# Performance work log

Measured on AMD Instinct MI355X. Metric: run time of the kernel, lower is better.

The kernel has to match this reference:

```python
import jax, jax.numpy as jnp
import numpy as np

N_POINTS = 1048576
N_LEVELS = 16
F = 2
BASE_RES = 16
FINEST_RES = 512
LOG2_HASH = 19
SIZES = [2 ** min(i + 1, LOG2_HASH) for i in range(N_LEVELS)]  # per-level table rows (powers of 2)
OFFS = np.concatenate([[0], np.cumsum(SIZES)]).astype(np.int64)  # static row offsets into packed table
TOTAL_ROWS = int(OFFS[-1])  # 131070
# hash primes from the torch module; uint32 wraparound matches int64 low-bit behavior
# because each table size is a power of two <= 2^19 < 2^32, so h % 2^k == low k bits.
P0, P1, P2, P3 = np.uint32(1), np.uint32(2654435761), np.uint32(29675113), np.uint32(123456789)
CORNERS = np.array([[0,0,0],[1,0,0],[0,1,0],[1,1,0],
                    [0,0,1],[1,0,1],[0,1,1],[1,1,1]], dtype=np.uint32)  # torch stacking order


def setup_inputs() -> dict:
    key = jax.random.key(0)
    k1, k2 = jax.random.split(key)
    coords = jax.random.uniform(k1, (N_POINTS, 3), dtype=jnp.float32, minval=-1.0, maxval=1.0)
    hash_init_scale = 0.001
    table = jax.random.uniform(k2, (TOTAL_ROWS, F), dtype=jnp.float32,
                               minval=-hash_init_scale, maxval=hash_init_scale)
    return {"coords": coords, "table": table}


def _encode(coords, table):
    corners = jnp.asarray(CORNERS)  # [8,3] uint32
    outs = []
    for level in range(N_LEVELS):
        res = min(BASE_RES * (2 ** level), FINEST_RES)
        cs = (coords + 1.0) * res           # [N,3]
        cf = jnp.floor(cs)
        frac = cs - cf                      # [N,3]
        base = cf.astype(jnp.uint32)        # coords >= -1 so floor >= 0
        c = base[None, :, :] + corners[:, None, :]   # [8,N,3]
        x, y, z = c[..., 0], c[..., 1], c[..., 2]
        h = x * P0
        h = h * P1 + y
        h = h * P2 + z
        h = h * P3
        h = (h & jnp.uint32(SIZES[level] - 1)).astype(jnp.int32)  # mod power-of-2 table size
        feats = table[int(OFFS[level]) + h]          # [8,N,F] gather
        tx = frac[..., 0:1]; ty = frac[..., 1:2]; tz = frac[..., 2:3]
        f = (feats[0] * (1 - tx) * (1 - ty) * (1 - tz)
             + feats[1] * tx * (1 - ty) * (1 - tz)
             + feats[2] * (1 - tx) * ty * (1 - tz)
             + feats[3] * tx * ty * (1 - tz)
             + feats[4] * (1 - tx) * (1 - ty) * tz
             + feats[5] * tx * (1 - ty) * tz
             + feats[6] * (1 - tx) * ty * tz
             + feats[7] * tx * ty * tz)              # [N,F]
        outs.append(f)
    return jnp.concatenate(outs, axis=-1)            # [N, N_LEVELS*F]


def reference(coords, table):
    return _encode(coords, table)
```

## Files before the change

### kernel.cpp

```cpp
#include <hip/hip_runtime.h>
#include <hip/hip_fp16.h>


#define BLOCK 1024
#define NBLOCKS 512
#define ITERS 16
#define STAGED_ROWS 32766
#define TBL_LDS_BYTES 131072
#define LDS_BYTES (TBL_LDS_BYTES + 16 * 128 * 8)

__device__ __forceinline__ float2 ldsRow(const unsigned* lds, unsigned idx) {
    unsigned u = lds[idx];
    __half2 h = *(__half2*)&u;
    return __half22float2(h);
}

#define PREP(FRES, HARR, WARR) \
    unsigned HARR[8]; float WARR[8]; { \
        const float csx = (px + 1.0f) * (FRES); \
        const float csy = (py + 1.0f) * (FRES); \
        const float csz = (pz + 1.0f) * (FRES); \
        const float cfx = floorf(csx), cfy = floorf(csy), cfz = floorf(csz); \
        const float tx = csx - cfx, ty = csy - cfy, tz = csz - cfz; \
        const unsigned hh = (unsigned)cfx * HA + (unsigned)cfy * HB + (unsigned)cfz * HC; \
        const float ux = 1.0f - tx, uy = 1.0f - ty, uz = 1.0f - tz; \
        WARR[0] = ux*uy*uz; WARR[1] = tx*uy*uz; WARR[2] = ux*ty*uz; WARR[3] = tx*ty*uz; \
        WARR[4] = ux*uy*tz; WARR[5] = tx*uy*tz; WARR[6] = ux*ty*tz; WARR[7] = tx*ty*tz; \
        HARR[0] = hh;           HARR[1] = hh + HA;           \
        HARR[2] = hh + HB;      HARR[3] = hh + HA + HB;      \
        HARR[4] = hh + HC;      HARR[5] = hh + HA + HC;      \
        HARR[6] = hh + HB + HC; HARR[7] = hh + HA + HB + HC; \
    }

#define GATHER_LDS(HARR, WARR, MASK, OFF, O0, O1) \
    { _Pragma("unroll") for (int c = 0; c < 8; ++c) { \
        float2 f = ldsRow(lds_tb, (OFF) + ((HARR[c]) & (MASK))); \
        (O0) += f.x * WARR[c]; (O1) += f.y * WARR[c]; } }

__global__ __launch_bounds__(BLOCK) void ngp_encode_kernel(
    const float* __restrict__ coords,
    const float* __restrict__ table,
    float* __restrict__ out)
{
    extern __shared__ unsigned char lds_raw[];
    unsigned* lds_tb = (unsigned*)lds_raw;
    float2* lds_t = (float2*)(lds_raw + TBL_LDS_BYTES);

    {
        const float4* __restrict__ t4 = (const float4*)table;
        uint2* __restrict__ l2 = (uint2*)lds_tb;
        for (int r = threadIdx.x; r < STAGED_ROWS / 2; r += BLOCK) {
            float4 v = t4[r];
            __half2 a = __floats2half2_rn(v.x, v.y);
            __half2 b = __floats2half2_rn(v.z, v.w);
            uint2 u;
            u.x = *(unsigned*)&a;
            u.y = *(unsigned*)&b;
            l2[r] = u;
        }
    }
    __syncthreads();

    constexpr unsigned P1 = 2654435761u, P2 = 29675113u, P3 = 123456789u;
    constexpr unsigned HA = P1 * P2 * P3;
    constexpr unsigned HB = P2 * P3;
    constexpr unsigned HC = P3;

    const float2* __restrict__ tb = (const float2*)table;
    float4* __restrict__ out4 = (float4*)out;

    const int wv   = __builtin_amdgcn_readfirstlane((int)(threadIdx.x >> 6));
    const int q    = wv & 7;
    const int g    = wv >> 3;
    const int lane = threadIdx.x & 63;
    const int pl   = g * 64 + lane;

    const int lA = q;
    const int lB = 15 - q;
    const unsigned maskA = (2u << lA) - 1u, offA = maskA - 1u;
    const unsigned maskB = (2u << lB) - 1u, offB = maskB - 1u;

    for (int it = 0; it < ITERS; ++it) {
        const int pbase = blockIdx.x * (ITERS * 128) + it * 128;
        const int p = pbase + pl;

        const float px = coords[3 * p + 0];
        const float py = coords[3 * p + 1];
        const float pz = coords[3 * p + 2];

        float oA0 = 0.0f, oA1 = 0.0f, oB0 = 0.0f, oB1 = 0.0f;

        if (q < 2) {
            PREP(512.0f, hB, wB)
            float2 gf0 = tb[offB + ((hB[0]) & maskB)];
            float2 gf1 = tb[offB + ((hB[1]) & maskB)];
            float2 gf2 = tb[offB + ((hB[2]) & maskB)];
            float2 gf3 = tb[offB + ((hB[3]) & maskB)];
            float2 gf4 = tb[offB + ((hB[4]) & maskB)];
            float2 gf5 = tb[offB + ((hB[5]) & maskB)];
            float2 gf6 = tb[offB + ((hB[6]) & maskB)];
            float2 gf7 = tb[offB + ((hB[7]) & maskB)];
            {
                const float fresA = (float)(16 << lA);
                PREP(fresA, hA, wA)
                GATHER_LDS(hA, wA, maskA, offA, oA0, oA1)
            }
            oB0 += gf0.x * wB[0]; oB1 += gf0.y * wB[0];
            oB0 += gf1.x * wB[1]; oB1 += gf1.y * wB[1];
            oB0 += gf2.x * wB[2]; oB1 += gf2.y * wB[2];
            oB0 += gf3.x * wB[3]; oB1 += gf3.y * wB[3];
            oB0 += gf4.x * wB[4]; oB1 += gf4.y * wB[4];
            oB0 += gf5.x * wB[5]; oB1 += gf5.y * wB[5];
            oB0 += gf6.x * wB[6]; oB1 += gf6.y * wB[6];
            oB0 += gf7.x * wB[7]; oB1 += gf7.y * wB[7];
        } else if (q < 5) {
            {
                const float fresA = (float)(16 << lA);
                PREP(fresA, hA, wA)
                GATHER_LDS(hA, wA, maskA, offA, oA0, oA1)
            }
            {
                PREP(512.0f, hB, wB)
                GATHER_LDS(hB, wB, maskB, offB, oB0, oB1)
            }
        } else {
            PREP(512.0f, hc, wc)
            GATHER_LDS(hc, wc, maskA, offA, oA0, oA1)
            GATHER_LDS(hc, wc, maskB, offB, oB0, oB1)
        }

        lds_t[lA * 128 + (pl ^ (lA & 14))] = make_float2(oA0, oA1);
        lds_t[lB * 128 + (pl ^ (lB & 14))] = make_float2(oB0, oB1);
        __syncthreads();
        {
            const int j  = threadIdx.x;
            const int lp = j >> 3, qq = j & 7;
            float2 a = lds_t[(2 * qq + 0) * 128 + (lp ^ (2 * qq))];
            float2 b = lds_t[(2 * qq + 1) * 128 + (lp ^ (2 * qq))];
            out4[(size_t)pbase * 8 + j] = make_float4(a.x, a.y, b.x, b.y);
        }
        __syncthreads();
    }
}

extern "C" void kernel_launch(void* const* d_in, const int* in_sizes, int n_in,
                              void* d_out, int out_size, void* d_ws, size_t ws_size,
                              hipStream_t stream) {
    const float* coords = (const float*)d_in[0];
    const float* table  = (const float*)d_in[1];
    float* out = (float*)d_out;

    hipFuncSetAttribute((const void*)ngp_encode_kernel,
                        hipFuncAttributeMaxDynamicSharedMemorySize,
                        LDS_BYTES);

    ngp_encode_kernel<<<NBLOCKS, BLOCK, LDS_BYTES, stream>>>(coords, table, out);
}
```

Measured before the change: 230.1 us.

## Double-buffer output staging, process two points per thread, shrink staged LDS table

Each iteration now handles 256 points, two per thread, and writes them into one of two alternating LDS output buffers. The store of the previous iteration's buffer overlaps the current compute, so only one barrier per iteration remains. The half-precision LDS table copy is halved to levels 0–12. This cuts per-block staging traffic, but level 13 now moves to direct global gathers, adding random global loads for one more wave group.

Result: no change. 228.6 us (-0.7%).

```diff
diff --git a/kernel.cpp b/kernel.cpp
--- a/kernel.cpp
+++ b/kernel.cpp
@@ -4,10 +4,11 @@
 
 #define BLOCK 1024
 #define NBLOCKS 512
-#define ITERS 16
-#define STAGED_ROWS 32766
-#define TBL_LDS_BYTES 131072
-#define LDS_BYTES (TBL_LDS_BYTES + 16 * 128 * 8)
+#define ITERS 8
+#define STAGED_ROWS 16382
+#define TBL_LDS_BYTES 65536
+#define BUF_F2 4096
+#define LDS_BYTES (TBL_LDS_BYTES + 2 * BUF_F2 * 8)
 
 __device__ __forceinline__ float2 ldsRow(const unsigned* lds, unsigned idx) {
     unsigned u = lds[idx];
@@ -44,7 +45,7 @@
 {
     extern __shared__ unsigned char lds_raw[];
     unsigned* lds_tb = (unsigned*)lds_raw;
-    float2* lds_t = (float2*)(lds_raw + TBL_LDS_BYTES);
+    float2* lds_buf = (float2*)(lds_raw + TBL_LDS_BYTES);
 
     {
         const float4* __restrict__ t4 = (const float4*)table;
@@ -73,73 +74,102 @@
     const int q    = wv & 7;
     const int g    = wv >> 3;
     const int lane = threadIdx.x & 63;
-    const int pl   = g * 64 + lane;
+    const int plb  = g * 64 + lane;
 
     const int lA = q;
     const int lB = 15 - q;
     const unsigned maskA = (2u << lA) - 1u, offA = maskA - 1u;
     const unsigned maskB = (2u << lB) - 1u, offB = maskB - 1u;
+    const unsigned xA = (unsigned)(lA & 14), xB = (unsigned)(lB & 14);
 
     for (int it = 0; it < ITERS; ++it) {
-        const int pbase = blockIdx.x * (ITERS * 128) + it * 128;
-        const int p = pbase + pl;
+        const int pbase = blockIdx.x * (ITERS * 256) + it * 256;
+        float2* bufW = lds_buf + (it & 1) * BUF_F2;
 
-        const float px = coords[3 * p + 0];
-        const float py = coords[3 * p + 1];
-        const float pz = coords[3 * p + 2];
+#pragma unroll
+        for (int half = 0; half < 2; ++half) {
+            const int pl = plb + half * 128;
+            const int p = pbase + pl;
+            const float px = coords[3 * p + 0];
+            const float py = coords[3 * p + 1];
+            const float pz = coords[3 * p + 2];
 
-        float oA0 = 0.0f, oA1 = 0.0f, oB0 = 0.0f, oB1 = 0.0f;
+            float oA0 = 0.0f, oA1 = 0.0f, oB0 = 0.0f, oB1 = 0.0f;
 
-        if (q < 2) {
-            PREP(512.0f, hB, wB)
-            float2 gf0 = tb[offB + ((hB[0]) & maskB)];
-            float2 gf1 = tb[offB + ((hB[1]) & maskB)];
-            float2 gf2 = tb[offB + ((hB[2]) & maskB)];
-            float2 gf3 = tb[offB + ((hB[3]) & maskB)];
-            float2 gf4 = tb[offB + ((hB[4]) & maskB)];
-            float2 gf5 = tb[offB + ((hB[5]) & maskB)];
-            float2 gf6 = tb[offB + ((hB[6]) & maskB)];
-            float2 gf7 = tb[offB + ((hB[7]) & maskB)];
-            {
-                const float fresA = (float)(16 << lA);
-                PREP(fresA, hA, wA)
-                GATHER_LDS(hA, wA, maskA, offA, oA0, oA1)
+            if (q < 3) {
+                PREP(512.0f, hB, wB)
+                float2 gf0 = tb[offB + ((hB[0]) & maskB)];
+                float2 gf1 = tb[offB + ((hB[1]) & maskB)];
+                float2 gf2 = tb[offB + ((hB[2]) & maskB)];
+                float2 gf3 = tb[offB + ((hB[3]) & maskB)];
+                float2 gf4 = tb[offB + ((hB[4]) & maskB)];
+                float2 gf5 = tb[offB + ((hB[5]) & maskB)];
+                float2 gf6 = tb[offB + ((hB[6]) & maskB)];
+                float2 gf7 = tb[offB + ((hB[7]) & maskB)];
+                {
+                    const float fresA = (float)(16 << lA);
+                    PREP(fresA, hA, wA)
+                    GATHER_LDS(hA, wA, maskA, offA, oA0, oA1)
+                }
+                oB0 += gf0.x * wB[0]; oB1 += gf0.y * wB[0];
+                oB0 += gf1.x * wB[1]; oB1 += gf1.y * wB[1];
+                oB0 += gf2.x * wB[2]; oB1 += gf2.y * wB[2];
+                oB0 += gf3.x * wB[3]; oB1 += gf3.y * wB[3];
+                oB0 += gf4.x * wB[4]; oB1 += gf4.y * wB[4];
+                oB0 += gf5.x * wB[5]; oB1 += gf5.y * wB[5];
+                oB0 += gf6.x * wB[6]; oB1 += gf6.y * wB[6];
+                oB0 += gf7.x * wB[7]; oB1 += gf7.y * wB[7];
+            } else if (q < 5) {
+                {
+                    const float fresA = (float)(16 << lA);
+                    PREP(fresA, hA, wA)
+                    GATHER_LDS(hA, wA, maskA, offA, oA0, oA1)
+                }
+                {
+                    PREP(512.0f, hB, wB)
+                    GATHER_LDS(hB, wB, maskB, offB, oB0, oB1)
+                }
+            } else {
+                PREP(512.0f, hc, wc)
+                GATHER_LDS(hc, wc, maskA, offA, oA0, oA1)
+                GATHER_LDS(hc, wc, maskB, offB, oB0, oB1)
             }
-            oB0 += gf0.x * wB[0]; oB1 += gf0.y * wB[0];
-            oB0 += gf1.x * wB[1]; oB1 += gf1.y * wB[1];
-            oB0 += gf2.x * wB[2]; oB1 += gf2.y * wB[2];
-            oB0 += gf3.x * wB[3]; oB1 += gf3.y * wB[3];
-            oB0 += gf4.x * wB[4]; oB1 += gf4.y * wB[4];
-            oB0 += gf5.x * wB[5]; oB1 += gf5.y * wB[5];
-            oB0 += gf6.x * wB[6]; oB1 += gf6.y * wB[6];
-            oB0 += gf7.x * wB[7]; oB1 += gf7.y * wB[7];
-        } else if (q < 5) {
-            {
-                const float fresA = (float)(16 << lA);
-                PREP(fresA, hA, wA)
-                GATHER_LDS(hA, wA, maskA, offA, oA0, oA1)
-            }
-            {
-                PREP(512.0f, hB, wB)
-                GATHER_LDS(hB, wB, maskB, offB, oB0, oB1)
-            }
-        } else {
-            PREP(512.0f, hc, wc)
-            GATHER_LDS(hc, wc, maskA, offA, oA0, oA1)
-            GATHER_LDS(hc, wc, maskB, offB, oB0, oB1)
+
+            bufW[lA * 256 + (pl ^ xA)] = make_float2(oA0, oA1);
+            bufW[lB * 256 + (pl ^ xB)] = make_float2(oB0, oB1);
         }
 
-        lds_t[lA * 128 + (pl ^ (lA & 14))] = make_float2(oA0, oA1);
-        lds_t[lB * 128 + (pl ^ (lB & 14))] = make_float2(oB0, oB1);
-        __syncthreads();
-        {
+        if (it > 0) {
+            const int sbase = pbase - 256;
+            const float2* bufR = lds_buf + ((it - 1) & 1) * BUF_F2;
             const int j  = threadIdx.x;
             const int lp = j >> 3, qq = j & 7;
-            float2 a = lds_t[(2 * qq + 0) * 128 + (lp ^ (2 * qq))];
-            float2 b = lds_t[(2 * qq + 1) * 128 + (lp ^ (2 * qq))];
-            out4[(size_t)pbase * 8 + j] = make_float4(a.x, a.y, b.x, b.y);
+            const unsigned xr = (unsigned)((2 * qq) & 14);
+#pragma unroll
+            for (int half = 0; half < 2; ++half) {
+                const int lpp = lp + half * 128;
+                float2 a = bufR[(2 * qq + 0) * 256 + (lpp ^ xr)];
+                float2 b = bufR[(2 * qq + 1) * 256 + (lpp ^ xr)];
+                out4[(size_t)(sbase + lpp) * 8 + qq] = make_float4(a.x, a.y, b.x, b.y);
+            }
         }
+
         __syncthreads();
+    }
+
+    {
+        const int sbase = blockIdx.x * (ITERS * 256) + (ITERS - 1) * 256;
+        const float2* bufR = lds_buf + ((ITERS - 1) & 1) * BUF_F2;
+        const int j  = threadIdx.x;
+        const int lp = j >> 3, qq = j & 7;
+        const unsigned xr = (unsigned)((2 * qq) & 14);
+#pragma unroll
+        for (int half = 0; half < 2; ++half) {
+            const int lpp = lp + half * 128;
+            float2 a = bufR[(2 * qq + 0) * 256 + (lpp ^ xr)];
+            float2 b = bufR[(2 * qq + 1) * 256 + (lpp ^ xr)];
+            out4[(size_t)(sbase + lpp) * 8 + qq] = make_float4(a.x, a.y, b.x, b.y);
+        }
     }
 }
 
```
